# Optimization experiments

Hardware: AMD Instinct MI355X
Metric: run time of the kernel (lower is better)

The kernel has to match this reference:

```python
import jax, jax.numpy as jnp
import numpy as np

EPS = 1e-6
LN_EPS = 1e-6

def _mlstm_parallel_stabilized(q, k, v, igate_preact, fgate_preact):
    # q,k,v: (B,NH,S,DH); igate_preact,fgate_preact: (B,NH,S,1)
    B, NH, S, DH = q.shape
    log_fg = jax.nn.log_sigmoid(fgate_preact[..., 0])            # (B,NH,S)
    cs = jnp.cumsum(log_fg, axis=-1)                             # (B,NH,S)
    # log decay matrix: entry (i,j) = cumsum_i - cumsum_j, lower-triangular (j<=i)
    fg_mat = cs[..., :, None] - cs[..., None, :]                 # (B,NH,S,S)
    mask = jnp.tril(jnp.ones((S, S), dtype=bool))
    log_D = jnp.where(mask, fg_mat + igate_preact[..., 0][..., None, :], -jnp.inf)
    max_log_D = jnp.max(log_D, axis=-1, keepdims=True)           # (B,NH,S,1)
    D = jnp.exp(log_D - max_log_D)                               # (B,NH,S,S)
    k_scaled = k / jnp.sqrt(jnp.float32(DH)).astype(k.dtype)
    qk = jnp.einsum('bhsd,bhtd->bhst', q, k_scaled)              # (B,NH,S,S)
    C = qk * D
    normalizer = jnp.maximum(jnp.abs(jnp.sum(C, axis=-1, keepdims=True)), jnp.exp(-max_log_D))
    C_norm = C / (normalizer + EPS)
    return jnp.einsum('bhst,bhtd->bhsd', C_norm, v)              # (B,NH,S,DH)

def _multihead_layernorm(x, weight):
    # x: (B,NH,S,DH), weight: (NH,DH); normalize over DH per head, no bias
    mu = jnp.mean(x, axis=-1, keepdims=True)
    var = jnp.mean(jnp.square(x - mu), axis=-1, keepdims=True)
    xn = (x - mu) * jax.lax.rsqrt(var + LN_EPS)
    return xn * weight[None, :, None, :]

def setup_inputs() -> dict:
    key = jax.random.key(0)
    ks = jax.random.split(key, 6)
    B, S, E, NH = 2, 2048, 1024, 8
    q = jax.random.normal(ks[0], (B, S, E), dtype=jnp.float32)
    k = jax.random.normal(ks[1], (B, S, E), dtype=jnp.float32)
    v = jax.random.normal(ks[2], (B, S, E), dtype=jnp.float32)
    igate_kernel = jnp.zeros((3 * E, NH), dtype=jnp.float32)
    igate_bias = 0.1 * jax.random.normal(ks[3], (NH,), dtype=jnp.float32)
    fgate_kernel = jnp.zeros((3 * E, NH), dtype=jnp.float32)
    fgate_bias = jnp.linspace(3.0, 6.0, NH, dtype=jnp.float32)
    outnorm_weight = jnp.ones((NH, E // NH), dtype=jnp.float32)
    return {"q": q, "k": k, "v": v,
            "igate_kernel": igate_kernel, "igate_bias": igate_bias,
            "fgate_kernel": fgate_kernel, "fgate_bias": fgate_bias,
            "outnorm_weight": outnorm_weight}

def reference(q, k, v, igate_kernel, igate_bias, fgate_kernel, fgate_bias, outnorm_weight):
    B, S, E = q.shape
    NH = igate_bias.shape[0]
    qkv = jnp.concatenate([q, k, v], axis=-1)                    # (B,S,3E)
    igate_preact = qkv @ igate_kernel + igate_bias               # (B,S,NH)
    fgate_preact = qkv @ fgate_kernel + fgate_bias               # (B,S,NH)
    qh = q.reshape(B, S, NH, -1).transpose(0, 2, 1, 3)           # (B,NH,S,DH)
    kh = k.reshape(B, S, NH, -1).transpose(0, 2, 1, 3)
    vh = v.reshape(B, S, NH, -1).transpose(0, 2, 1, 3)
    ig = igate_preact.transpose(0, 2, 1)[..., None]              # (B,NH,S,1)
    fg = fgate_preact.transpose(0, 2, 1)[..., None]
    h = _mlstm_parallel_stabilized(qh, kh, vh, ig, fg)           # (B,NH,S,DH)
    h_norm = _multihead_layernorm(h, outnorm_weight)
    return h_norm.transpose(0, 2, 1, 3).reshape(B, S, -1)        # (B,S,E)
```

## Files before the change

kernel.cpp:

```cpp
#include <hip/hip_runtime.h>
#include <math.h>

#define S_LEN 2048
#define E_DIM 1024
#define NHEAD 8
#define DHEAD 128

typedef short bf16x8 __attribute__((ext_vector_type(8)));
typedef float f32x4 __attribute__((ext_vector_type(4)));
typedef unsigned int u32x4 __attribute__((ext_vector_type(4)));
typedef unsigned int u32x2 __attribute__((ext_vector_type(2)));

constexpr float RSQ_DH  = 0.08838834764831843f;
constexpr float LNRSQ   = -2.4260151319598084f;
constexpr float EPS_NORM = 1e-6f;
constexpr float LN_EPS_C = 1e-6f;

__device__ inline unsigned bfpair(float lo, float hi) {
  unsigned a = __builtin_bit_cast(unsigned, lo);
  unsigned b = __builtin_bit_cast(unsigned, hi);
  a = (a + 0x7fffu + ((a >> 16) & 1u)) >> 16;
  b = (b + 0x7fffu + ((b >> 16) & 1u)) >> 16;
  return a | (b << 16);
}

__device__ inline unsigned cvtpk(float lo, float hi) {
  unsigned r;
  asm("v_cvt_pk_bf16_f32 %0, %1, %2" : "=v"(r) : "v"(lo), "v"(hi));
  return r;
}

__device__ inline void gload_lds16(const void* g, void* lds) {
  __builtin_amdgcn_global_load_lds(
      (const __attribute__((address_space(1))) unsigned int*)g,
      (__attribute__((address_space(3))) unsigned int*)lds, 16, 0, 0);
}
__device__ inline void gload_lds4(const void* g, void* lds) {
  __builtin_amdgcn_global_load_lds(
      (const __attribute__((address_space(1))) unsigned int*)g,
      (__attribute__((address_space(3))) unsigned int*)lds, 4, 0, 0);
}

__global__ __launch_bounds__(256) void gates_fused(
    const float* __restrict__ q, const float* __restrict__ k, const float* __restrict__ v,
    const float* __restrict__ Wi, const float* __restrict__ bi,
    const float* __restrict__ Wf, const float* __restrict__ bf,
    float* __restrict__ ig_pre, float* __restrict__ fg_pre,
    unsigned short* __restrict__ kb) {
  const int t = threadIdx.x;
  const int row0 = blockIdx.x * 4;
  const int b = row0 >> 11;
  const int s0 = row0 & 2047;
  float p[4][16];
#pragma unroll
  for (int rr = 0; rr < 4; ++rr)
#pragma unroll
    for (int c = 0; c < 16; ++c) p[rr][c] = 0.f;

#pragma unroll
  for (int i = 0; i < 3; ++i) {
    const float* base = (i == 0) ? q : (i == 1) ? k : v;
    float xs[4][4];
#pragma unroll
    for (int rr = 0; rr < 4; ++rr) {
      const float4 xv = *(const float4*)(base + (size_t)(row0 + rr) * E_DIM + t * 4);
      xs[rr][0] = xv.x; xs[rr][1] = xv.y; xs[rr][2] = xv.z; xs[rr][3] = xv.w;
    }
#pragma unroll
    for (int j = 0; j < 4; ++j) {
      const int ge = i * E_DIM + t * 4 + j;
      const float4 wiA = *(const float4*)(Wi + (size_t)ge * 8);
      const float4 wiB = *(const float4*)(Wi + (size_t)ge * 8 + 4);
      const float4 wfA = *(const float4*)(Wf + (size_t)ge * 8);
      const float4 wfB = *(const float4*)(Wf + (size_t)ge * 8 + 4);
      const float wv16[16] = {wiA.x, wiA.y, wiA.z, wiA.w, wiB.x, wiB.y, wiB.z, wiB.w,
                              wfA.x, wfA.y, wfA.z, wfA.w, wfB.x, wfB.y, wfB.z, wfB.w};
#pragma unroll
      for (int rr = 0; rr < 4; ++rr) {
        const float x = xs[rr][j];
#pragma unroll
        for (int c = 0; c < 16; ++c) p[rr][c] += x * wv16[c];
      }
    }
    if (i == 1 && kb != nullptr) {
      const int h = (t * 4) >> 7, d = (t * 4) & 127;
#pragma unroll
      for (int rr = 0; rr < 4; ++rr) {
        u32x2 pk;
        pk.x = bfpair(xs[rr][0], xs[rr][1]);
        pk.y = bfpair(xs[rr][2], xs[rr][3]);
        *(u32x2*)(kb + (((size_t)b * NHEAD + h) * S_LEN + (s0 + rr)) * DHEAD + d) = pk;
      }
    }
  }

#pragma unroll
  for (int rr = 0; rr < 4; ++rr)
#pragma unroll
    for (int c = 0; c < 16; ++c) {
      float val = p[rr][c];
      val += __shfl_xor(val, 1);
      val += __shfl_xor(val, 2);
      val += __shfl_xor(val, 4);
      val += __shfl_xor(val, 8);
      val += __shfl_xor(val, 16);
      val += __shfl_xor(val, 32);
      p[rr][c] = val;
    }
  __shared__ float sred[4][4][16];
  const int wid = t >> 6, lane = t & 63;
  if (lane == 0) {
#pragma unroll
    for (int rr = 0; rr < 4; ++rr)
#pragma unroll
      for (int c = 0; c < 16; ++c) sred[wid][rr][c] = p[rr][c];
  }
  __syncthreads();
  if (t < 64) {
    const int rr = t >> 4, c = t & 15;
    float sum = sred[0][rr][c] + sred[1][rr][c] + sred[2][rr][c] + sred[3][rr][c];
    const int h = c & 7;
    const int row = row0 + rr;
    const int bb = row / S_LEN, s = row % S_LEN;
    if (c < 8) ig_pre[((size_t)bb * NHEAD + h) * S_LEN + s] = sum + bi[h];
    else       fg_pre[((size_t)bb * NHEAD + h) * S_LEN + s] = sum + bf[h];
  }
}

__global__ __launch_bounds__(256) void vtrans(const float* __restrict__ v,
                                              unsigned short* __restrict__ vtb) {
  __shared__ unsigned int tile[128][36];
  const int bid = blockIdx.x;
  const int bh = bid >> 5, st = bid & 31;
  const int b = bh >> 3, h = bh & 7;
  const int s0 = st * 64;
  const int t = threadIdx.x;
#pragma unroll
  for (int i = 0; i < 4; ++i) {
    const int task = t + 256 * i;
    const int sp = task & 31, dq = task >> 5;
    const float* src = v + ((size_t)b * S_LEN + s0 + 2 * sp) * E_DIM + h * DHEAD + dq * 4;
    const float4 r0 = *(const float4*)(src);
    const float4 r1 = *(const float4*)(src + E_DIM);
    tile[dq * 4 + 0][sp] = bfpair(r0.x, r1.x);
    tile[dq * 4 + 1][sp] = bfpair(r0.y, r1.y);
    tile[dq * 4 + 2][sp] = bfpair(r0.z, r1.z);
    tile[dq * 4 + 3][sp] = bfpair(r0.w, r1.w);
  }
  __syncthreads();
#pragma unroll
  for (int i = 0; i < 2; ++i) {
    const int task = t + 256 * i;
    const int d = task >> 2, c4 = task & 3;
    u32x4 w0, w1;
    w0.x = tile[d][c4 * 8 + 0]; w0.y = tile[d][c4 * 8 + 1];
    w0.z = tile[d][c4 * 8 + 2]; w0.w = tile[d][c4 * 8 + 3];
    w1.x = tile[d][c4 * 8 + 4]; w1.y = tile[d][c4 * 8 + 5];
    w1.z = tile[d][c4 * 8 + 6]; w1.w = tile[d][c4 * 8 + 7];
    unsigned short* dst = vtb + ((size_t)bh * DHEAD + d) * S_LEN + s0 + c4 * 16;
    *(u32x4*)(dst)     = w0;
    *(u32x4*)(dst + 8) = w1;
  }
}

__global__ __launch_bounds__(256) void scan_kernel(
    const float* __restrict__ ig_pre, const float* __restrict__ fg_pre,
    float* __restrict__ cs_out, float* __restrict__ g_out, float* __restrict__ gmax_out,
    float g_add) {
  const int bhh = blockIdx.x;
  const int t = threadIdx.x;
  const size_t base = (size_t)bhh * S_LEN;
  float vals[8];
  float run = 0.f;
#pragma unroll
  for (int i = 0; i < 8; ++i) {
    const float x = fg_pre[base + t * 8 + i];
    const float lf = fminf(x, 0.f) - log1pf(__expf(-fabsf(x)));
    run += lf;
    vals[i] = run;
  }
  __shared__ float sums[256];
  sums[t] = run;
  __syncthreads();
  for (int off = 1; off < 256; off <<= 1) {
    const float other = (t >= off) ? sums[t - off] : 0.f;
    __syncthreads();
    sums[t] += other;
    __syncthreads();
  }
  const float prefix = (t > 0) ? sums[t - 1] : 0.f;
  float g_loc[8], gm_loc[8];
  float lmax = -3.4e38f;
#pragma unroll
  for (int i = 0; i < 8; ++i) {
    const float csv = vals[i] + prefix;
    vals[i] = csv;
    const float gg = ig_pre[base + t * 8 + i] - csv;
    g_loc[i] = gg;
    lmax = fmaxf(lmax, gg);
    gm_loc[i] = lmax;
  }
  __shared__ float maxs[256];
  maxs[t] = lmax;
  __syncthreads();
  for (int off = 1; off < 256; off <<= 1) {
    const float other = (t >= off) ? maxs[t - off] : -3.4e38f;
    __syncthreads();
    maxs[t] = fmaxf(maxs[t], other);
    __syncthreads();
  }
  const float pmax = (t > 0) ? maxs[t - 1] : -3.4e38f;
#pragma unroll
  for (int i = 0; i < 8; ++i) {
    cs_out[base + t * 8 + i]   = vals[i];
    g_out[base + t * 8 + i]    = g_loc[i] + g_add;
    gmax_out[base + t * 8 + i] = fmaxf(gm_loc[i], pmax);
  }
}

__global__ __launch_bounds__(512, 4) void mlstm_mfma8(
    const unsigned short* __restrict__ kb, const unsigned short* __restrict__ vtb,
    const float* __restrict__ q,
    const float* __restrict__ cs, const float* __restrict__ garr, const float* __restrict__ gmax,
    const float* __restrict__ wgt, float* __restrict__ out) {
  __shared__ __align__(16) unsigned char kbuf[4][8192];
  __shared__ __align__(16) unsigned char vbuf[4][8192];
  __shared__ float g_sh[4][32];
  __shared__ float den_sh[4][64];

  const int bid = blockIdx.x;
  int qb;
  if (bid < 256) qb = 31 - (bid >> 4);
  else           qb = (bid - 256) >> 4;
  const int g16 = bid & 15;
  const int bh = 2 * (g16 & 7) + (g16 >> 3);
  const int b = bh >> 3, h = bh & 7;
  const int t = threadIdx.x;
  const int w = t >> 6;
  const int ig = w & 3;
  const int tp = w >> 2;
  const int l = t & 63;
  const int r = l & 15;
  const int qq = l >> 4;
  const size_t bhS = (size_t)bh * S_LEN;

  const int gr = qb * 64 + 4 * r + ig;
  const float gm_lane = gmax[bhS + gr];

  bf16x8 qfrag[4];
  {
    const float* qrow = q + ((size_t)b * S_LEN + gr) * E_DIM + h * DHEAD;
#pragma unroll
    for (int c = 0; c < 4; ++c) {
      const float4 f0 = *(const float4*)(qrow + 32 * c + 8 * qq);
      const float4 f1 = *(const float4*)(qrow + 32 * c + 8 * qq + 4);
      u32x4 u;
      u.x = bfpair(f0.x, f0.y); u.y = bfpair(f0.z, f0.w);
      u.z = bfpair(f1.x, f1.y); u.w = bfpair(f1.z, f1.w);
      qfrag[c] = __builtin_bit_cast(bf16x8, u);
    }
  }

  f32x4 o[8];
#pragma unroll
  for (int n = 0; n < 8; ++n) o[n] = (f32x4){0.f, 0.f, 0.f, 0.f};
  float den_p = 0.f;

  const unsigned short* kt = kb + bhS * DHEAD;
  const unsigned short* vt = vtb + (size_t)bh * DHEAD * S_LEN;

  auto stage = [&](int pair, int set) {
    const int j0 = pair * 64 + tp * 32;
    const int bi = set * 2 + tp;
#pragma unroll
    for (int a = 0; a < 2; ++a) {
      const int m = ig * 128 + a * 64 + l;
      const int u = m ^ ((m >> 4) & 7);
      gload_lds16(kt + ((size_t)(j0 + (u >> 4))) * DHEAD + (u & 15) * 8,
                  &kbuf[bi][(ig * 128 + a * 64) * 16]);
    }
#pragma unroll
    for (int a = 0; a < 2; ++a) {
      const int m = ig * 128 + a * 64 + l;
      const int u = m ^ ((m >> 3) & 7);
      gload_lds16(vt + (size_t)(u >> 2) * S_LEN + j0 + (u & 3) * 8,
                  &vbuf[bi][(ig * 128 + a * 64) * 16]);
    }
    if (l < 32) gload_lds4(garr + bhS + j0 + l, &g_sh[bi][0]);
  };

  auto body = [&](int j0, int bi, bool diag) {
    __builtin_amdgcn_s_setprio(1);
    f32x4 st0 = {0, 0, 0, 0}, st1 = {0, 0, 0, 0};
#pragma unroll
    for (int c = 0; c < 4; ++c) {
      const int u0 = ((r)      * 16 + 4 * c + qq) ^ (r & 7);
      const int u1 = ((16 + r) * 16 + 4 * c + qq) ^ (r & 7);
      bf16x8 ka0 = *(const bf16x8*)&kbuf[bi][u0 * 16];
      bf16x8 ka1 = *(const bf16x8*)&kbuf[bi][u1 * 16];
      st0 = __builtin_amdgcn_mfma_f32_16x16x32_bf16(ka0, qfrag[c], st0, 0, 0, 0);
      st1 = __builtin_amdgcn_mfma_f32_16x16x32_bf16(ka1, qfrag[c], st1, 0, 0, 0);
    }
    __builtin_amdgcn_s_setprio(0);

    unsigned P0[2], P1[2];
    {
      float wv[4];
#pragma unroll
      for (int m = 0; m < 4; ++m) {
        const int jl = 4 * qq + m;
        float ww = st0[m] * __expf(g_sh[bi][jl] - gm_lane);
        if (diag && (j0 + jl > gr)) ww = 0.f;
        wv[m] = ww; den_p += ww;
      }
      P0[0] = cvtpk(wv[0], wv[1]); P0[1] = cvtpk(wv[2], wv[3]);
#pragma unroll
      for (int m = 0; m < 4; ++m) {
        const int jl = 16 + 4 * qq + m;
        float ww = st1[m] * __expf(g_sh[bi][jl] - gm_lane);
        if (diag && (j0 + jl > gr)) ww = 0.f;
        wv[m] = ww; den_p += ww;
      }
      P1[0] = cvtpk(wv[0], wv[1]); P1[1] = cvtpk(wv[2], wv[3]);
    }

    unsigned A0[4];
#pragma unroll
    for (int m = 0; m < 4; ++m) {
      const int srcl = r + 16 * (2 * (qq & 1) + (m >> 1));
      const unsigned x0 = (unsigned)__shfl((int)P0[m & 1], srcl);
      const unsigned x1 = (unsigned)__shfl((int)P1[m & 1], srcl);
      A0[m] = (qq < 2) ? x0 : x1;
    }
    u32x4 ua;
    ua.x = A0[0]; ua.y = A0[1]; ua.z = A0[2]; ua.w = A0[3];
    const bf16x8 pa = __builtin_bit_cast(bf16x8, ua);

    __builtin_amdgcn_s_setprio(1);
#pragma unroll
    for (int n = 0; n < 8; ++n) {
      const int ud = (16 * n + r) * 4 + qq;
      const int up = ud ^ ((ud >> 3) & 7);
      bf16x8 vb = *(const bf16x8*)&vbuf[bi][up * 16];
      o[n] = __builtin_amdgcn_mfma_f32_16x16x32_bf16(pa, vb, o[n], 0, 0, 0);
    }
    __builtin_amdgcn_s_setprio(0);
  };

  stage(0, 0);
  for (int p = 0; p < qb; ++p) {
    stage(p + 1, (p + 1) & 1);
    asm volatile("s_waitcnt vmcnt(5)" ::: "memory");
    __builtin_amdgcn_sched_barrier(0);
    __syncthreads();
    body(p * 64 + tp * 32, (p & 1) * 2 + tp, false);
    __syncthreads();
  }
  asm volatile("s_waitcnt vmcnt(0)" ::: "memory");
  __builtin_amdgcn_sched_barrier(0);
  __syncthreads();
  body(qb * 64 + tp * 32, (qb & 1) * 2 + tp, true);

  float* osh = (float*)&kbuf[0][0];
  __syncthreads();
  if (tp == 1) {
#pragma unroll
    for (int n = 0; n < 8; ++n)
      *(f32x4*)&osh[(((n << 2) + ig) * 64 + l) * 4] = o[n];
    den_sh[ig][l] = den_p;
  }
  __syncthreads();
  if (tp == 0) {
    den_p += den_sh[ig][l];
#pragma unroll
    for (int n = 0; n < 8; ++n)
      o[n] += *(const f32x4*)&osh[(((n << 2) + ig) * 64 + l) * 4];

    float den_f = den_p;
    den_f += __shfl_xor(den_f, 16);
    den_f += __shfl_xor(den_f, 32);

    const float* wrow = wgt + h * DHEAD;
    float wv_n[8];
#pragma unroll
    for (int n = 0; n < 8; ++n) wv_n[n] = wrow[16 * n + r];

#pragma unroll
    for (int m = 0; m < 4; ++m) {
      const int iloc = 4 * qq + m;
      const float den_o = __shfl(den_f, iloc);
      const int grow = qb * 64 + 4 * iloc + ig;
      const float csg = cs[bhS + grow];
      const float gmg = gmax[bhS + grow];
      const float norm = fmaxf(fabsf(den_o), __expf(-(csg + gmg))) + EPS_NORM;
      const float inv = 1.f / norm;
      float hv[8];
      float s1 = 0.f, s2 = 0.f;
#pragma unroll
      for (int n = 0; n < 8; ++n) {
        hv[n] = o[n][m] * inv;
        s1 += hv[n]; s2 += hv[n] * hv[n];
      }
      s1 += __shfl_xor(s1, 1); s1 += __shfl_xor(s1, 2);
      s1 += __shfl_xor(s1, 4); s1 += __shfl_xor(s1, 8);
      s2 += __shfl_xor(s2, 1); s2 += __shfl_xor(s2, 2);
      s2 += __shfl_xor(s2, 4); s2 += __shfl_xor(s2, 8);
      const float mu  = s1 * (1.f / 128.f);
      const float var = s2 * (1.f / 128.f) - mu * mu;
      const float rstd = rsqrtf(var + LN_EPS_C);
      float* orow = out + ((size_t)b * S_LEN + grow) * E_DIM + h * DHEAD;
#pragma unroll
      for (int n = 0; n < 8; ++n)
        orow[16 * n + r] = (hv[n] - mu) * rstd * wv_n[n];
    }
  }
}

__global__ __launch_bounds__(256) void mlstm_mfma(
    const float* __restrict__ q, const float* __restrict__ k, const float* __restrict__ v,
    const float* __restrict__ cs, const float* __restrict__ garr, const float* __restrict__ gmax,
    const float* __restrict__ wgt, float* __restrict__ out) {
  __shared__ unsigned short k_lds[32][136];
  __shared__ unsigned int   vt_u32[128][20];
  __shared__ unsigned int   xch[4][16][20];
  __shared__ float          g_sh[32];

  const int bid = blockIdx.x;
  int qt;
  if (bid < 256) qt = 31 - (bid >> 4);
  else           qt = (bid - 256) >> 4;
  const int bh = bid & 15;
  const int b = bh >> 3, h = bh & 7;
  const int t = threadIdx.x;
  const int w = t >> 6;
  const int l = t & 63;
  const int r = l & 15;
  const int qq = l >> 4;
  const size_t bhS = (size_t)bh * S_LEN;

  const int gr = qt * 64 + 4 * r + w;
  const float gm_lane = gmax[bhS + gr];

  bf16x8 qfrag[4];
  {
    const float* qrow = q + ((size_t)b * S_LEN + gr) * E_DIM + h * DHEAD;
#pragma unroll
    for (int c = 0; c < 4; ++c) {
      const float4 f0 = *(const float4*)(qrow + 32 * c + 8 * qq);
      const float4 f1 = *(const float4*)(qrow + 32 * c + 8 * qq + 4);
      u32x4 u;
      u.x = bfpair(f0.x, f0.y); u.y = bfpair(f0.z, f0.w);
      u.z = bfpair(f1.x, f1.y); u.w = bfpair(f1.z, f1.w);
      qfrag[c] = __builtin_bit_cast(bf16x8, u);
    }
  }

  f32x4 o[8];
#pragma unroll
  for (int n = 0; n < 8; ++n) o[n] = (f32x4){0.f, 0.f, 0.f, 0.f};
  float den_p = 0.f;

  const int kj = t >> 3, ks = t & 7;
  const int vjp = t & 15, vds = t >> 4;

  const int ntiles = 2 * qt + 2;
  for (int jt = 0; jt < ntiles; ++jt) {
    const int j0 = jt * 32;
    {
      const float* src = k + ((size_t)b * S_LEN + j0 + kj) * E_DIM + h * DHEAD + ks * 16;
      float4 f0 = *(const float4*)(src);
      float4 f1 = *(const float4*)(src + 4);
      float4 f2 = *(const float4*)(src + 8);
      float4 f3 = *(const float4*)(src + 12);
      u32x4 ua, ub;
      ua.x = bfpair(f0.x, f0.y); ua.y = bfpair(f0.z, f0.w);
      ua.z = bfpair(f1.x, f1.y); ua.w = bfpair(f1.z, f1.w);
      ub.x = bfpair(f2.x, f2.y); ub.y = bfpair(f2.z, f2.w);
      ub.z = bfpair(f3.x, f3.y); ub.w = bfpair(f3.z, f3.w);
      *(u32x4*)&k_lds[kj][ks * 16]     = ua;
      *(u32x4*)&k_lds[kj][ks * 16 + 8] = ub;
    }
    {
      const float* s0 = v + ((size_t)b * S_LEN + j0 + 2 * vjp) * E_DIM + h * DHEAD + vds * 8;
      const float* s1 = s0 + E_DIM;
      float4 a0 = *(const float4*)(s0);
      float4 a1 = *(const float4*)(s0 + 4);
      float4 b0 = *(const float4*)(s1);
      float4 b1 = *(const float4*)(s1 + 4);
      vt_u32[vds * 8 + 0][vjp] = bfpair(a0.x, b0.x);
      vt_u32[vds * 8 + 1][vjp] = bfpair(a0.y, b0.y);
      vt_u32[vds * 8 + 2][vjp] = bfpair(a0.z, b0.z);
      vt_u32[vds * 8 + 3][vjp] = bfpair(a0.w, b0.w);
      vt_u32[vds * 8 + 4][vjp] = bfpair(a1.x, b1.x);
      vt_u32[vds * 8 + 5][vjp] = bfpair(a1.y, b1.y);
      vt_u32[vds * 8 + 6][vjp] = bfpair(a1.z, b1.z);
      vt_u32[vds * 8 + 7][vjp] = bfpair(a1.w, b1.w);
    }
    if (t < 32) g_sh[t] = garr[bhS + j0 + t];
    __syncthreads();

    f32x4 st0 = {0, 0, 0, 0}, st1 = {0, 0, 0, 0};
#pragma unroll
    for (int c = 0; c < 4; ++c) {
      bf16x8 ka0 = *(const bf16x8*)&k_lds[r][32 * c + 8 * qq];
      bf16x8 ka1 = *(const bf16x8*)&k_lds[16 + r][32 * c + 8 * qq];
      st0 = __builtin_amdgcn_mfma_f32_16x16x32_bf16(ka0, qfrag[c], st0, 0, 0, 0);
      st1 = __builtin_amdgcn_mfma_f32_16x16x32_bf16(ka1, qfrag[c], st1, 0, 0, 0);
    }

    const bool diag = (jt >= 2 * qt);
    float wv0[4], wv1[4];
#pragma unroll
    for (int reg = 0; reg < 4; ++reg) {
      const int jl0 = 4 * qq + reg, jl1 = 16 + 4 * qq + reg;
      const float e0 = __expf(g_sh[jl0] - gm_lane);
      const float e1 = __expf(g_sh[jl1] - gm_lane);
      float w0 = st0[reg] * RSQ_DH * e0;
      float w1 = st1[reg] * RSQ_DH * e1;
      if (diag) {
        if (j0 + jl0 > gr) w0 = 0.f;
        if (j0 + jl1 > gr) w1 = 0.f;
      }
      wv0[reg] = w0; wv1[reg] = w1;
      den_p += w0 + w1;
    }

    u32x2 p0, p1;
    p0.x = bfpair(wv0[0], wv0[1]); p0.y = bfpair(wv0[2], wv0[3]);
    p1.x = bfpair(wv1[0], wv1[1]); p1.y = bfpair(wv1[2], wv1[3]);
    *(u32x2*)&xch[w][r][2 * qq]     = p0;
    *(u32x2*)&xch[w][r][8 + 2 * qq] = p1;
    __builtin_amdgcn_wave_barrier();
    bf16x8 pa = *(const bf16x8*)&xch[w][r][4 * qq];
    __builtin_amdgcn_wave_barrier();

#pragma unroll
    for (int n = 0; n < 8; ++n) {
      bf16x8 vb = *(const bf16x8*)&vt_u32[16 * n + r][4 * qq];
      o[n] = __builtin_amdgcn_mfma_f32_16x16x32_bf16(pa, vb, o[n], 0, 0, 0);
    }
    __syncthreads();
  }

  float den_f = den_p;
  den_f += __shfl_xor(den_f, 16);
  den_f += __shfl_xor(den_f, 32);

  const float* wrow = wgt + h * DHEAD;
  float wv_n[8];
#pragma unroll
  for (int n = 0; n < 8; ++n) wv_n[n] = wrow[16 * n + r];

#pragma unroll
  for (int reg = 0; reg < 4; ++reg) {
    const int iloc = 4 * qq + reg;
    const float den_o = __shfl(den_f, iloc);
    const int grow = qt * 64 + 4 * iloc + w;
    const float csg = cs[bhS + grow];
    const float gmg = gmax[bhS + grow];
    const float norm = fmaxf(fabsf(den_o), __expf(-(csg + gmg))) + EPS_NORM;
    const float inv = 1.f / norm;
    float hv[8];
    float s1 = 0.f, s2 = 0.f;
#pragma unroll
    for (int n = 0; n < 8; ++n) {
      hv[n] = o[n][reg] * inv;
      s1 += hv[n]; s2 += hv[n] * hv[n];
    }
    s1 += __shfl_xor(s1, 1); s1 += __shfl_xor(s1, 2);
    s1 += __shfl_xor(s1, 4); s1 += __shfl_xor(s1, 8);
    s2 += __shfl_xor(s2, 1); s2 += __shfl_xor(s2, 2);
    s2 += __shfl_xor(s2, 4); s2 += __shfl_xor(s2, 8);
    const float mu  = s1 * (1.f / 128.f);
    const float var = s2 * (1.f / 128.f) - mu * mu;
    const float rstd = rsqrtf(var + LN_EPS_C);
    float* orow = out + ((size_t)b * S_LEN + grow) * E_DIM + h * DHEAD;
#pragma unroll
    for (int n = 0; n < 8; ++n)
      orow[16 * n + r] = (hv[n] - mu) * rstd * wv_n[n];
  }
}

extern "C" void kernel_launch(void* const* d_in, const int* in_sizes, int n_in,
                              void* d_out, int out_size, void* d_ws, size_t ws_size,
                              hipStream_t stream) {
  (void)in_sizes; (void)n_in; (void)out_size;
  const float* q   = (const float*)d_in[0];
  const float* k   = (const float*)d_in[1];
  const float* v   = (const float*)d_in[2];
  const float* Wi  = (const float*)d_in[3];
  const float* bi  = (const float*)d_in[4];
  const float* Wf  = (const float*)d_in[5];
  const float* bf  = (const float*)d_in[6];
  const float* wgt = (const float*)d_in[7];
  float* out = (float*)d_out;
  float* ws  = (float*)d_ws;
  const int BNS = 2 * NHEAD * S_LEN;
  float* ig_pre = ws;
  float* fg_pre = ws + (size_t)BNS;
  float* cs     = ws + (size_t)2 * BNS;
  float* gv     = ws + (size_t)3 * BNS;
  float* gmaxs  = ws + (size_t)4 * BNS;
  unsigned short* kb  = (unsigned short*)(ws + (size_t)5 * BNS);
  unsigned short* vtb = kb + (size_t)16 * S_LEN * DHEAD;

  const size_t need = (size_t)5 * BNS * 4 + (size_t)2 * 16 * S_LEN * DHEAD * 2;

  if (ws_size >= need) {
    gates_fused<<<1024, 256, 0, stream>>>(q, k, v, Wi, bi, Wf, bf, ig_pre, fg_pre, kb);
    vtrans<<<512, 256, 0, stream>>>(v, vtb);
    scan_kernel<<<16, 256, 0, stream>>>(ig_pre, fg_pre, cs, gv, gmaxs, LNRSQ);
    mlstm_mfma8<<<512, 512, 0, stream>>>(kb, vtb, q, cs, gv, gmaxs, wgt, out);
  } else {
    gates_fused<<<1024, 256, 0, stream>>>(q, k, v, Wi, bi, Wf, bf, ig_pre, fg_pre, nullptr);
    scan_kernel<<<16, 256, 0, stream>>>(ig_pre, fg_pre, cs, gv, gmaxs, 0.0f);
    mlstm_mfma<<<512, 256, 0, stream>>>(q, k, v, cs, gv, gmaxs, wgt, out);
  }
}
```

Before: 106.6 us.

## Process two query rows per wave in mLSTM kernel and use wave-shuffle scans

The main attention kernel drops from 8 to 4 waves per block, and each wave now holds two query-row fragments. Every K and V fragment read from LDS feeds two MFMAs, which halves LDS read traffic per MFMA, and the exp factor is shared between the rows through a precomputed ratio. The cost is roughly double the accumulator registers per wave, fewer waves to hide latency, and each wave now issues twice as many staging loads. The scan kernel also replaces its shared-memory Hillis-Steele loops, which needed many __syncthreads, with wavefront shuffle scans plus a small cross-wave combine.

```diff
diff --git a/kernel.cpp b/kernel.cpp
--- a/kernel.cpp
+++ b/kernel.cpp
@@ -169,6 +169,7 @@
     float g_add) {
   const int bhh = blockIdx.x;
   const int t = threadIdx.x;
+  const int lane = t & 63, wid = t >> 6;
   const size_t base = (size_t)bhh * S_LEN;
   float vals[8];
   float run = 0.f;
@@ -179,16 +180,21 @@
     run += lf;
     vals[i] = run;
   }
-  __shared__ float sums[256];
-  sums[t] = run;
+  float ws = run;
+#pragma unroll
+  for (int off = 1; off < 64; off <<= 1) {
+    const float v = __shfl_up(ws, off);
+    if (lane >= off) ws += v;
+  }
+  __shared__ float wsum[4];
+  if (lane == 63) wsum[wid] = ws;
   __syncthreads();
-  for (int off = 1; off < 256; off <<= 1) {
-    const float other = (t >= off) ? sums[t - off] : 0.f;
-    __syncthreads();
-    sums[t] += other;
-    __syncthreads();
-  }
-  const float prefix = (t > 0) ? sums[t - 1] : 0.f;
+  float wpre = 0.f;
+#pragma unroll
+  for (int kk = 0; kk < 4; ++kk)
+    if (kk < wid) wpre += wsum[kk];
+  const float prefix = wpre + (ws - run);
+
   float g_loc[8], gm_loc[8];
   float lmax = -3.4e38f;
 #pragma unroll
@@ -200,16 +206,23 @@
     lmax = fmaxf(lmax, gg);
     gm_loc[i] = lmax;
   }
-  __shared__ float maxs[256];
-  maxs[t] = lmax;
+  float wm = lmax;
+#pragma unroll
+  for (int off = 1; off < 64; off <<= 1) {
+    const float v = __shfl_up(wm, off);
+    if (lane >= off) wm = fmaxf(wm, v);
+  }
+  __shared__ float wmax[4];
+  if (lane == 63) wmax[wid] = wm;
   __syncthreads();
-  for (int off = 1; off < 256; off <<= 1) {
-    const float other = (t >= off) ? maxs[t - off] : -3.4e38f;
-    __syncthreads();
-    maxs[t] = fmaxf(maxs[t], other);
-    __syncthreads();
-  }
-  const float pmax = (t > 0) ? maxs[t - 1] : -3.4e38f;
+  float mpre = -3.4e38f;
+#pragma unroll
+  for (int kk = 0; kk < 4; ++kk)
+    if (kk < wid) mpre = fmaxf(mpre, wmax[kk]);
+  float excl = __shfl_up(wm, 1);
+  if (lane == 0) excl = -3.4e38f;
+  const float pmax = fmaxf(mpre, excl);
+
 #pragma unroll
   for (int i = 0; i < 8; ++i) {
     cs_out[base + t * 8 + i]   = vals[i];
@@ -218,7 +231,7 @@
   }
 }
 
-__global__ __launch_bounds__(512, 4) void mlstm_mfma8(
+__global__ __launch_bounds__(256) void mlstm_mfma9(
     const unsigned short* __restrict__ kb, const unsigned short* __restrict__ vtb,
     const float* __restrict__ q,
     const float* __restrict__ cs, const float* __restrict__ garr, const float* __restrict__ gmax,
@@ -237,34 +250,43 @@
   const int b = bh >> 3, h = bh & 7;
   const int t = threadIdx.x;
   const int w = t >> 6;
-  const int ig = w & 3;
-  const int tp = w >> 2;
+  const int iw = w & 1;
+  const int tp = w >> 1;
   const int l = t & 63;
   const int r = l & 15;
   const int qq = l >> 4;
   const size_t bhS = (size_t)bh * S_LEN;
 
-  const int gr = qb * 64 + 4 * r + ig;
-  const float gm_lane = gmax[bhS + gr];
-
-  bf16x8 qfrag[4];
+  const int grA = qb * 64 + 4 * r + 2 * iw;
+  const int grB = grA + 1;
+  const float gmA = gmax[bhS + grA];
+  const float gmB = gmax[bhS + grB];
+  const float rAB = __expf(gmA - gmB);
+
+  bf16x8 qfA[4], qfB[4];
   {
-    const float* qrow = q + ((size_t)b * S_LEN + gr) * E_DIM + h * DHEAD;
+    const float* qrowA = q + ((size_t)b * S_LEN + grA) * E_DIM + h * DHEAD;
+    const float* qrowB = q + ((size_t)b * S_LEN + grB) * E_DIM + h * DHEAD;
 #pragma unroll
     for (int c = 0; c < 4; ++c) {
-      const float4 f0 = *(const float4*)(qrow + 32 * c + 8 * qq);
-      const float4 f1 = *(const float4*)(qrow + 32 * c + 8 * qq + 4);
+      float4 f0 = *(const float4*)(qrowA + 32 * c + 8 * qq);
+      float4 f1 = *(const float4*)(qrowA + 32 * c + 8 * qq + 4);
       u32x4 u;
       u.x = bfpair(f0.x, f0.y); u.y = bfpair(f0.z, f0.w);
       u.z = bfpair(f1.x, f1.y); u.w = bfpair(f1.z, f1.w);
-      qfrag[c] = __builtin_bit_cast(bf16x8, u);
-    }
-  }
-
-  f32x4 o[8];
-#pragma unroll
-  for (int n = 0; n < 8; ++n) o[n] = (f32x4){0.f, 0.f, 0.f, 0.f};
-  float den_p = 0.f;
+      qfA[c] = __builtin_bit_cast(bf16x8, u);
+      f0 = *(const float4*)(qrowB + 32 * c + 8 * qq);
+      f1 = *(const float4*)(qrowB + 32 * c + 8 * qq + 4);
+      u.x = bfpair(f0.x, f0.y); u.y = bfpair(f0.z, f0.w);
+      u.z = bfpair(f1.x, f1.y); u.w = bfpair(f1.z, f1.w);
+      qfB[c] = __builtin_bit_cast(bf16x8, u);
+    }
+  }
+
+  f32x4 oA[8], oB[8];
+#pragma unroll
+  for (int n = 0; n < 8; ++n) { oA[n] = (f32x4){0,0,0,0}; oB[n] = (f32x4){0,0,0,0}; }
+  float denA = 0.f, denB = 0.f;
 
   const unsigned short* kt = kb + bhS * DHEAD;
   const unsigned short* vt = vtb + (size_t)bh * DHEAD * S_LEN;
@@ -273,68 +295,87 @@
     const int j0 = pair * 64 + tp * 32;
     const int bi = set * 2 + tp;
 #pragma unroll
-    for (int a = 0; a < 2; ++a) {
-      const int m = ig * 128 + a * 64 + l;
+    for (int a = 0; a < 4; ++a) {
+      const int m = iw * 256 + a * 64 + l;
       const int u = m ^ ((m >> 4) & 7);
       gload_lds16(kt + ((size_t)(j0 + (u >> 4))) * DHEAD + (u & 15) * 8,
-                  &kbuf[bi][(ig * 128 + a * 64) * 16]);
-    }
-#pragma unroll
-    for (int a = 0; a < 2; ++a) {
-      const int m = ig * 128 + a * 64 + l;
+                  &kbuf[bi][(iw * 256 + a * 64) * 16]);
+    }
+#pragma unroll
+    for (int a = 0; a < 4; ++a) {
+      const int m = iw * 256 + a * 64 + l;
       const int u = m ^ ((m >> 3) & 7);
       gload_lds16(vt + (size_t)(u >> 2) * S_LEN + j0 + (u & 3) * 8,
-                  &vbuf[bi][(ig * 128 + a * 64) * 16]);
+                  &vbuf[bi][(iw * 256 + a * 64) * 16]);
     }
     if (l < 32) gload_lds4(garr + bhS + j0 + l, &g_sh[bi][0]);
   };
 
   auto body = [&](int j0, int bi, bool diag) {
     __builtin_amdgcn_s_setprio(1);
-    f32x4 st0 = {0, 0, 0, 0}, st1 = {0, 0, 0, 0};
+    f32x4 sA0 = {0,0,0,0}, sA1 = {0,0,0,0}, sB0 = {0,0,0,0}, sB1 = {0,0,0,0};
 #pragma unroll
     for (int c = 0; c < 4; ++c) {
       const int u0 = ((r)      * 16 + 4 * c + qq) ^ (r & 7);
       const int u1 = ((16 + r) * 16 + 4 * c + qq) ^ (r & 7);
       bf16x8 ka0 = *(const bf16x8*)&kbuf[bi][u0 * 16];
       bf16x8 ka1 = *(const bf16x8*)&kbuf[bi][u1 * 16];
-      st0 = __builtin_amdgcn_mfma_f32_16x16x32_bf16(ka0, qfrag[c], st0, 0, 0, 0);
-      st1 = __builtin_amdgcn_mfma_f32_16x16x32_bf16(ka1, qfrag[c], st1, 0, 0, 0);
+      sA0 = __builtin_amdgcn_mfma_f32_16x16x32_bf16(ka0, qfA[c], sA0, 0, 0, 0);
+      sB0 = __builtin_amdgcn_mfma_f32_16x16x32_bf16(ka0, qfB[c], sB0, 0, 0, 0);
+      sA1 = __builtin_amdgcn_mfma_f32_16x16x32_bf16(ka1, qfA[c], sA1, 0, 0, 0);
+      sB1 = __builtin_amdgcn_mfma_f32_16x16x32_bf16(ka1, qfB[c], sB1, 0, 0, 0);
     }
     __builtin_amdgcn_s_setprio(0);
 
-    unsigned P0[2], P1[2];
+    unsigned PA0[2], PA1[2], PB0[2], PB1[2];
     {
-      float wv[4];
+      float wa[4], wb[4];
 #pragma unroll
       for (int m = 0; m < 4; ++m) {
         const int jl = 4 * qq + m;
-        float ww = st0[m] * __expf(g_sh[bi][jl] - gm_lane);
-        if (diag && (j0 + jl > gr)) ww = 0.f;
-        wv[m] = ww; den_p += ww;
+        const float e = __expf(g_sh[bi][jl] - gmA);
+        float a = sA0[m] * e;
+        float bq = sB0[m] * e * rAB;
+        if (diag) {
+          if (j0 + jl > grA) a = 0.f;
+          if (j0 + jl > grB) bq = 0.f;
+        }
+        wa[m] = a; wb[m] = bq; denA += a; denB += bq;
       }
-      P0[0] = cvtpk(wv[0], wv[1]); P0[1] = cvtpk(wv[2], wv[3]);
+      PA0[0] = cvtpk(wa[0], wa[1]); PA0[1] = cvtpk(wa[2], wa[3]);
+      PB0[0] = cvtpk(wb[0], wb[1]); PB0[1] = cvtpk(wb[2], wb[3]);
 #pragma unroll
       for (int m = 0; m < 4; ++m) {
         const int jl = 16 + 4 * qq + m;
-        float ww = st1[m] * __expf(g_sh[bi][jl] - gm_lane);
-        if (diag && (j0 + jl > gr)) ww = 0.f;
-        wv[m] = ww; den_p += ww;
+        const float e = __expf(g_sh[bi][jl] - gmA);
+        float a = sA1[m] * e;
+        float bq = sB1[m] * e * rAB;
+        if (diag) {
+          if (j0 + jl > grA) a = 0.f;
+          if (j0 + jl > grB) bq = 0.f;
+        }
+        wa[m] = a; wb[m] = bq; denA += a; denB += bq;
       }
-      P1[0] = cvtpk(wv[0], wv[1]); P1[1] = cvtpk(wv[2], wv[3]);
-    }
-
-    unsigned A0[4];
+      PA1[0] = cvtpk(wa[0], wa[1]); PA1[1] = cvtpk(wa[2], wa[3]);
+      PB1[0] = cvtpk(wb[0], wb[1]); PB1[1] = cvtpk(wb[2], wb[3]);
+    }
+
+    unsigned AA[4], AB[4];
 #pragma unroll
     for (int m = 0; m < 4; ++m) {
       const int srcl = r + 16 * (2 * (qq & 1) + (m >> 1));
-      const unsigned x0 = (unsigned)__shfl((int)P0[m & 1], srcl);
-      const unsigned x1 = (unsigned)__shfl((int)P1[m & 1], srcl);
-      A0[m] = (qq < 2) ? x0 : x1;
-    }
-    u32x4 ua;
-    ua.x = A0[0]; ua.y = A0[1]; ua.z = A0[2]; ua.w = A0[3];
-    const bf16x8 pa = __builtin_bit_cast(bf16x8, ua);
+      const unsigned a0 = (unsigned)__shfl((int)PA0[m & 1], srcl);
+      const unsigned a1 = (unsigned)__shfl((int)PA1[m & 1], srcl);
+      const unsigned b0 = (unsigned)__shfl((int)PB0[m & 1], srcl);
+      const unsigned b1 = (unsigned)__shfl((int)PB1[m & 1], srcl);
+      AA[m] = (qq < 2) ? a0 : a1;
+      AB[m] = (qq < 2) ? b0 : b1;
+    }
+    u32x4 ua, ub;
+    ua.x = AA[0]; ua.y = AA[1]; ua.z = AA[2]; ua.w = AA[3];
+    ub.x = AB[0]; ub.y = AB[1]; ub.z = AB[2]; ub.w = AB[3];
+    const bf16x8 paA = __builtin_bit_cast(bf16x8, ua);
+    const bf16x8 paB = __builtin_bit_cast(bf16x8, ub);
 
     __builtin_amdgcn_s_setprio(1);
 #pragma unroll
@@ -342,7 +383,8 @@
       const int ud = (16 * n + r) * 4 + qq;
       const int up = ud ^ ((ud >> 3) & 7);
       bf16x8 vb = *(const bf16x8*)&vbuf[bi][up * 16];
-      o[n] = __builtin_amdgcn_mfma_f32_16x16x32_bf16(pa, vb, o[n], 0, 0, 0);
+      oA[n] = __builtin_amdgcn_mfma_f32_16x16x32_bf16(paA, vb, oA[n], 0, 0, 0);
+      oB[n] = __builtin_amdgcn_mfma_f32_16x16x32_bf16(paB, vb, oB[n], 0, 0, 0);
     }
     __builtin_amdgcn_s_setprio(0);
   };
@@ -350,7 +392,7 @@
   stage(0, 0);
   for (int p = 0; p < qb; ++p) {
     stage(p + 1, (p + 1) & 1);
-    asm volatile("s_waitcnt vmcnt(5)" ::: "memory");
+    asm volatile("s_waitcnt vmcnt(9)" ::: "memory");
     __builtin_amdgcn_sched_barrier(0);
     __syncthreads();
     body(p * 64 + tp * 32, (p & 1) * 2 + tp, false);
@@ -363,22 +405,29 @@
 
   float* osh = (float*)&kbuf[0][0];
   __syncthreads();
+  const int xsw = (r & 7) << 2;
   if (tp == 1) {
 #pragma unroll
-    for (int n = 0; n < 8; ++n)
-      *(f32x4*)&osh[(((n << 2) + ig) * 64 + l) * 4] = o[n];
-    den_sh[ig][l] = den_p;
+    for (int n = 0; n < 8; ++n) {
+      const int i0 = ((((16 * n + r) * 2 + iw) * 2 + 0) * 16 + 4 * qq) ^ xsw;
+      const int i1 = ((((16 * n + r) * 2 + iw) * 2 + 1) * 16 + 4 * qq) ^ xsw;
+      *(f32x4*)&osh[i0] = oA[n];
+      *(f32x4*)&osh[i1] = oB[n];
+    }
+    den_sh[iw * 2 + 0][l] = denA;
+    den_sh[iw * 2 + 1][l] = denB;
   }
   __syncthreads();
   if (tp == 0) {
-    den_p += den_sh[ig][l];
-#pragma unroll
-    for (int n = 0; n < 8; ++n)
-      o[n] += *(const f32x4*)&osh[(((n << 2) + ig) * 64 + l) * 4];
-
-    float den_f = den_p;
-    den_f += __shfl_xor(den_f, 16);
-    den_f += __shfl_xor(den_f, 32);
+    denA += den_sh[iw * 2 + 0][l];
+    denB += den_sh[iw * 2 + 1][l];
+#pragma unroll
+    for (int n = 0; n < 8; ++n) {
+      const int i0 = ((((16 * n + r) * 2 + iw) * 2 + 0) * 16 + 4 * qq) ^ xsw;
+      const int i1 = ((((16 * n + r) * 2 + iw) * 2 + 1) * 16 + 4 * qq) ^ xsw;
+      oA[n] += *(const f32x4*)&osh[i0];
+      oB[n] += *(const f32x4*)&osh[i1];
+    }
 
     const float* wrow = wgt + h * DHEAD;
     float wv_n[8];
@@ -386,32 +435,38 @@
     for (int n = 0; n < 8; ++n) wv_n[n] = wrow[16 * n + r];
 
 #pragma unroll
-    for (int m = 0; m < 4; ++m) {
-      const int iloc = 4 * qq + m;
-      const float den_o = __shfl(den_f, iloc);
-      const int grow = qb * 64 + 4 * iloc + ig;
-      const float csg = cs[bhS + grow];
-      const float gmg = gmax[bhS + grow];
-      const float norm = fmaxf(fabsf(den_o), __expf(-(csg + gmg))) + EPS_NORM;
-      const float inv = 1.f / norm;
-      float hv[8];
-      float s1 = 0.f, s2 = 0.f;
-#pragma unroll
-      for (int n = 0; n < 8; ++n) {
-        hv[n] = o[n][m] * inv;
-        s1 += hv[n]; s2 += hv[n] * hv[n];
+    for (int fg = 0; fg < 2; ++fg) {
+      float den_f = (fg == 0) ? denA : denB;
+      den_f += __shfl_xor(den_f, 16);
+      den_f += __shfl_xor(den_f, 32);
+#pragma unroll
+      for (int m = 0; m < 4; ++m) {
+        const int iloc = 4 * qq + m;
+        const float den_o = __shfl(den_f, iloc);
+        const int grow = qb * 64 + 4 * iloc + 2 * iw + fg;
+        const float csg = cs[bhS + grow];
+        const float gmg = gmax[bhS + grow];
+        const float norm = fmaxf(fabsf(den_o), __expf(-(csg + gmg))) + EPS_NORM;
+        const float inv = 1.f / norm;
+        float hv[8];
+        float s1 = 0.f, s2 = 0.f;
+#pragma unroll
+        for (int n = 0; n < 8; ++n) {
+          hv[n] = ((fg == 0) ? oA[n][m] : oB[n][m]) * inv;
+          s1 += hv[n]; s2 += hv[n] * hv[n];
+        }
+        s1 += __shfl_xor(s1, 1); s1 += __shfl_xor(s1, 2);
+        s1 += __shfl_xor(s1, 4); s1 += __shfl_xor(s1, 8);
+        s2 += __shfl_xor(s2, 1); s2 += __shfl_xor(s2, 2);
+        s2 += __shfl_xor(s2, 4); s2 += __shfl_xor(s2, 8);
+        const float mu  = s1 * (1.f / 128.f);
+        const float var = s2 * (1.f / 128.f) - mu * mu;
+        const float rstd = rsqrtf(var + LN_EPS_C);
+        float* orow = out + ((size_t)b * S_LEN + grow) * E_DIM + h * DHEAD;
+#pragma unroll
+        for (int n = 0; n < 8; ++n)
+          orow[16 * n + r] = (hv[n] - mu) * rstd * wv_n[n];
       }
-      s1 += __shfl_xor(s1, 1); s1 += __shfl_xor(s1, 2);
-      s1 += __shfl_xor(s1, 4); s1 += __shfl_xor(s1, 8);
-      s2 += __shfl_xor(s2, 1); s2 += __shfl_xor(s2, 2);
-      s2 += __shfl_xor(s2, 4); s2 += __shfl_xor(s2, 8);
-      const float mu  = s1 * (1.f / 128.f);
-      const float var = s2 * (1.f / 128.f) - mu * mu;
-      const float rstd = rsqrtf(var + LN_EPS_C);
-      float* orow = out + ((size_t)b * S_LEN + grow) * E_DIM + h * DHEAD;
-#pragma unroll
-      for (int n = 0; n < 8; ++n)
-        orow[16 * n + r] = (hv[n] - mu) * rstd * wv_n[n];
     }
   }
 }
@@ -610,7 +665,7 @@
     gates_fused<<<1024, 256, 0, stream>>>(q, k, v, Wi, bi, Wf, bf, ig_pre, fg_pre, kb);
     vtrans<<<512, 256, 0, stream>>>(v, vtb);
     scan_kernel<<<16, 256, 0, stream>>>(ig_pre, fg_pre, cs, gv, gmaxs, LNRSQ);
-    mlstm_mfma8<<<512, 512, 0, stream>>>(kb, vtb, q, cs, gv, gmaxs, wgt, out);
+    mlstm_mfma9<<<512, 256, 0, stream>>>(kb, vtb, q, cs, gv, gmaxs, wgt, out);
   } else {
     gates_fused<<<1024, 256, 0, stream>>>(q, k, v, Wi, bi, Wf, bf, ig_pre, fg_pre, nullptr);
     scan_kernel<<<16, 256, 0, stream>>>(ig_pre, fg_pre, cs, gv, gmaxs, 0.0f);
```

After: 102.1 us. 1.04x faster.
